# Performance work log

Measured on AMD Instinct MI355X. Metric: run time of the kernel, lower is better.

## Reference

```python
import jax, jax.numpy as jnp
import numpy as np

MIN_NORM = 1e-15
PROJ_EPS = 4e-3  # float32 boundary eps used by hgcn PoincareBall.proj
N_NODES = 100000
BATCH = 32
MAX_COMMENTS = 50
C = 1.0  # comment_curvature


def _norm(x):
    return jnp.maximum(jnp.sqrt(jnp.sum(x * x, axis=-1, keepdims=True)), MIN_NORM)


def _artanh(x):
    return jnp.arctanh(jnp.clip(x, -1.0 + 1e-7, 1.0 - 1e-7))


def proj(x, c):
    n = _norm(x)
    maxnorm = (1.0 - PROJ_EPS) / jnp.sqrt(c)
    return jnp.where(n > maxnorm, x / n * maxnorm, x)


def expmap0(u, c):
    sqc = jnp.sqrt(c)
    un = _norm(u)
    return jnp.tanh(sqc * un) * u / (sqc * un)


def logmap0(p, c):
    sqc = jnp.sqrt(c)
    pn = _norm(p)
    return _artanh(sqc * pn) * p / (sqc * pn)


def mobius_add(x, y, c):
    x2 = jnp.sum(x * x, axis=-1, keepdims=True)
    y2 = jnp.sum(y * y, axis=-1, keepdims=True)
    xy = jnp.sum(x * y, axis=-1, keepdims=True)
    num = (1.0 + 2.0 * c * xy + c * y2) * x + (1.0 - c * x2) * y
    den = 1.0 + 2.0 * c * xy + (c ** 2) * x2 * y2
    return num / jnp.maximum(den, MIN_NORM)


def mobius_matvec(m, x, c):
    sqc = jnp.sqrt(c)
    xn = _norm(x)
    mx = x @ m.T  # [N, out]
    mxn = _norm(mx)
    res = jnp.tanh(mxn / xn * _artanh(sqc * xn)) * mx / (mxn * sqc)
    zero = jnp.all(mx == 0.0, axis=-1, keepdims=True)
    return jnp.where(zero, jnp.zeros_like(res), res)


def hgcn_layer(x, W, b, row, col, n_nodes, c):
    # HypLinear (dropout off / eval mode)
    mv = proj(mobius_matvec(W, x, c), c)
    hyp_bias = proj(expmap0(b[None, :], c), c)
    h = proj(mobius_add(mv, hyp_bias, c), c)
    # HypAgg: tangent-space sparse aggregation adj @ log0(h)
    ht = logmap0(h, c)
    agg = jax.ops.segment_sum(ht[col], row, num_segments=n_nodes)
    h = proj(expmap0(agg, c), c)
    # HypAct with tanh, c_in == c_out
    at = jnp.tanh(logmap0(h, c))
    return proj(expmap0(at, c), c)


def setup_inputs() -> dict:
    key = jax.random.key(0)
    ks = jax.random.split(key, 8)
    E = 1600000
    x = jax.random.normal(ks[0], (N_NODES, 256), dtype=jnp.float32) * 0.1
    edge_row = jax.random.randint(ks[1], (E,), 0, N_NODES, dtype=jnp.int32)
    edge_col = jax.random.randint(ks[2], (E,), 0, N_NODES, dtype=jnp.int32)
    seg_ids = jax.random.randint(ks[3], (N_NODES,), 0, BATCH * MAX_COMMENTS, dtype=jnp.int32)
    W1 = jax.random.normal(ks[4], (128, 256), dtype=jnp.float32) * 0.05
    b1 = jax.random.normal(ks[5], (128,), dtype=jnp.float32) * 0.05
    W2 = jax.random.normal(ks[6], (128, 128), dtype=jnp.float32) * 0.05
    b2 = jax.random.normal(ks[7], (128,), dtype=jnp.float32) * 0.05
    return {"x": x, "edge_row": edge_row, "edge_col": edge_col, "seg_ids": seg_ids,
            "W1": W1, "b1": b1, "W2": W2, "b2": b2}


def reference(x, edge_row, edge_col, seg_ids, W1, b1, W2, b2):
    c = jnp.float32(C)
    # map Euclidean inputs to the Poincare ball (proj_tan0 is identity)
    h = proj(expmap0(x, c), c)
    h = hgcn_layer(h, W1, b1, edge_row, edge_col, N_NODES, c)
    h = hgcn_layer(h, W2, b2, edge_row, edge_col, N_NODES, c)
    # back to tangent space
    h = logmap0(proj(h, c), c)  # [N, hidden]
    # per-subgraph mean pooling (dgl.mean_nodes over node_subgraphs)
    n_seg = BATCH * MAX_COMMENTS
    ssum = jax.ops.segment_sum(h, seg_ids, num_segments=n_seg)
    cnt = jax.ops.segment_sum(jnp.ones((N_NODES,), h.dtype), seg_ids, num_segments=n_seg)
    mean = ssum / jnp.maximum(cnt, 1.0)[:, None]  # empty segments -> zero rows (padding)
    agg = proj(expmap0(mean, c), c)
    return agg.reshape(BATCH, MAX_COMMENTS, -1)
```

## Files before the change

kernel.cpp:

```cpp
#include <hip/hip_runtime.h>


#define MAXN 0.996f
#define CLIPV 0.9999999f
#define MINNORM 1e-15f

typedef __attribute__((ext_vector_type(8))) short  short8;
typedef __attribute__((ext_vector_type(4))) float  f32x4;
typedef __attribute__((ext_vector_type(4))) unsigned short us4;

__device__ __forceinline__ float wave_sum(float v) {
#pragma unroll
  for (int o = 32; o > 0; o >>= 1) v += __shfl_xor(v, o);
  return v;
}
__device__ __forceinline__ float sum16(float v) {
#pragma unroll
  for (int o = 8; o > 0; o >>= 1) v += __shfl_xor(v, o);
  return v;
}

__device__ __forceinline__ unsigned short f2bf(float f) {
  unsigned int u = __float_as_uint(f);
  u = (u + 0x7FFFu + ((u >> 16) & 1u)) >> 16;
  return (unsigned short)u;
}
__device__ __forceinline__ float bf_lo(unsigned int u) {
  return __uint_as_float(u << 16);
}
__device__ __forceinline__ float bf_hi(unsigned int u) {
  return __uint_as_float(u & 0xFFFF0000u);
}

__global__ void bias_kernel(const float* __restrict__ b1i,
                            const float* __restrict__ b2i,
                            float* __restrict__ hb1, float* __restrict__ hb2,
                            float* __restrict__ y21, float* __restrict__ y22) {
  const float* b = blockIdx.x ? b2i : b1i;
  float* hb = blockIdx.x ? hb2 : hb1;
  float* y2o = blockIdx.x ? y22 : y21;
  int lane = threadIdx.x;
  float b0 = b[lane], b1 = b[lane + 64];
  float ssq = wave_sum(b0 * b0 + b1 * b1);
  float un = fmaxf(sqrtf(ssq), MINNORM);
  float t = tanhf(un);
  float s = t / un;
  float n = t;
  if (n > MAXN) { s *= MAXN / n; n = MAXN; }
  hb[lane] = s * b0;
  hb[lane + 64] = s * b1;
  if (lane == 0) y2o[0] = n * n;
}

__global__ void hist_kernel(const int* __restrict__ keys, int* __restrict__ cnt,
                            int n) {
  int e = blockIdx.x * 256 + threadIdx.x;
  if (e < n) atomicAdd(&cnt[keys[e]], 1);
}

__global__ __launch_bounds__(256) void scan_kernel(const int* __restrict__ in,
                                                   int* __restrict__ out,
                                                   int* __restrict__ bsum, int n) {
  __shared__ int sh[256];
  int t = threadIdx.x;
  int base = blockIdx.x * 1024 + t * 4;
  int v0 = 0, v1 = 0, v2 = 0, v3 = 0;
  if (base + 0 < n) v0 = in[base + 0];
  if (base + 1 < n) v1 = in[base + 1];
  if (base + 2 < n) v2 = in[base + 2];
  if (base + 3 < n) v3 = in[base + 3];
  int s = v0 + v1 + v2 + v3;
  sh[t] = s;
  __syncthreads();
  int run = s;
  for (int o = 1; o < 256; o <<= 1) {
    int add = (t >= o) ? sh[t - o] : 0;
    __syncthreads();
    run += add;
    sh[t] = run;
    __syncthreads();
  }
  int excl = run - s;
  if (base + 0 < n) out[base + 0] = excl;
  if (base + 1 < n) out[base + 1] = excl + v0;
  if (base + 2 < n) out[base + 2] = excl + v0 + v1;
  if (base + 3 < n) out[base + 3] = excl + v0 + v1 + v2;
  if (t == 255 && bsum) bsum[blockIdx.x] = run;
}

__global__ void scan_add_kernel(int* __restrict__ pre, const int* __restrict__ boff,
                                int n, int total) {
  int i = blockIdx.x * 256 + threadIdx.x;
  if (i < n) pre[i] += boff[blockIdx.x >> 2];
  if (i == 0) pre[n] = total;
}

__global__ __launch_bounds__(256) void sscan_kernel(const int* __restrict__ in,
                                                    int* __restrict__ out, int n) {
  __shared__ int sh[256];
  int t = threadIdx.x;
  int base = t * 8;
  int v[8];
  int s = 0;
#pragma unroll
  for (int i = 0; i < 8; i++) {
    v[i] = (base + i < n) ? in[base + i] : 0;
    s += v[i];
  }
  sh[t] = s;
  __syncthreads();
  int run = s;
  for (int o = 1; o < 256; o <<= 1) {
    int add = (t >= o) ? sh[t - o] : 0;
    __syncthreads();
    run += add;
    sh[t] = run;
    __syncthreads();
  }
  int running = run - s;
#pragma unroll
  for (int i = 0; i < 8; i++) {
    if (base + i < n) out[base + i] = running;
    running += v[i];
  }
  if (t == 255) out[n] = running;
}

__global__ void fill_kernel(const int* __restrict__ erow, const int* __restrict__ ecol,
                            const int* __restrict__ rowptr, int* __restrict__ fill,
                            int* __restrict__ colidx, int E) {
  int e = blockIdx.x * 256 + threadIdx.x;
  if (e >= E) return;
  int r = erow[e];
  int pos = rowptr[r] + atomicAdd(&fill[r], 1);
  colidx[pos] = ecol[e];
}

__global__ void sfill_kernel(const int* __restrict__ seg,
                             const int* __restrict__ sptr, int* __restrict__ sfil,
                             int* __restrict__ snode, int M) {
  int i = blockIdx.x * 256 + threadIdx.x;
  if (i >= M) return;
  int s = seg[i];
  int pos = sptr[s] + atomicAdd(&sfil[s], 1);
  snode[pos] = i;
}

template <bool L1>
__global__ __launch_bounds__(256) void gemm_fused(const void* __restrict__ Xv,
                                                  const float* __restrict__ Wt,
                                                  const float* __restrict__ hb_g,
                                                  const float* __restrict__ y2_g,
                                                  const float* __restrict__ xnin,
                                                  unsigned short* __restrict__ HT,
                                                  int M, int K) {
  constexpr int GS = 128 * 16 + 16;
  __shared__ alignas(16) char smem[8 * GS];
  __shared__ float hbs[128];
  __shared__ float redS[128][2], redD[128][2];
  __shared__ float rowA[128], rowB[128];
  __shared__ float fsh[128], xsh[128];
  char* sA = smem;
  char* sB = smem + 4 * GS;
  int tid = threadIdx.x;
  int lane = tid & 63;
  int w = tid >> 6;
  int wr = w >> 1, wc = w & 1;
  int m0 = blockIdx.x * 128;

  if (tid < 128) hbs[tid] = hb_g[tid];

  float ssqr[4] = {0.f, 0.f, 0.f, 0.f};
  f32x4 acc[4][4] = {};
  for (int k0 = 0; k0 < K; k0 += 32) {
#pragma unroll
    for (int j = 0; j < 4; j++) {
      int i = tid + 256 * j;
      int row = i >> 3;
      int koff = (i & 7) * 4;
      int gm = m0 + row;
      us4 av;
      if constexpr (L1) {
        if (gm < M) {
          float4 v = *reinterpret_cast<const float4*>(
              &((const float*)Xv)[(size_t)gm * K + k0 + koff]);
          ssqr[j] += v.x * v.x + v.y * v.y + v.z * v.z + v.w * v.w;
          av[0] = f2bf(v.x); av[1] = f2bf(v.y); av[2] = f2bf(v.z); av[3] = f2bf(v.w);
        } else { av[0] = 0; av[1] = 0; av[2] = 0; av[3] = 0; }
      } else {
        if (gm < M) av = *reinterpret_cast<const us4*>(
            &((const unsigned short*)Xv)[(size_t)gm * K + k0 + koff]);
        else { av[0] = 0; av[1] = 0; av[2] = 0; av[3] = 0; }
      }
      *reinterpret_cast<us4*>(&sA[(koff >> 3) * GS + row * 16 + (koff & 7) * 2]) = av;
      float4 wv = *reinterpret_cast<const float4*>(&Wt[(size_t)row * K + k0 + koff]);
      us4 bv;
      bv[0] = f2bf(wv.x); bv[1] = f2bf(wv.y); bv[2] = f2bf(wv.z); bv[3] = f2bf(wv.w);
      *reinterpret_cast<us4*>(&sB[(koff >> 3) * GS + row * 16 + (koff & 7) * 2]) = bv;
    }
    __syncthreads();
    int g = lane >> 4, r = lane & 15;
    short8 af[4], bfr[4];
#pragma unroll
    for (int mb = 0; mb < 4; mb++)
      af[mb] = *reinterpret_cast<const short8*>(
          &sA[g * GS + (wr * 64 + mb * 16 + r) * 16]);
#pragma unroll
    for (int nb = 0; nb < 4; nb++)
      bfr[nb] = *reinterpret_cast<const short8*>(
          &sB[g * GS + (wc * 64 + nb * 16 + r) * 16]);
#pragma unroll
    for (int mb = 0; mb < 4; mb++)
#pragma unroll
      for (int nb = 0; nb < 4; nb++)
        acc[mb][nb] = __builtin_amdgcn_mfma_f32_16x16x32_bf16(
            af[mb], bfr[nb], acc[mb][nb], 0, 0, 0);
    __syncthreads();
  }

  if constexpr (L1) {
#pragma unroll
    for (int j = 0; j < 4; j++) {
      float s = ssqr[j];
      s += __shfl_xor(s, 1); s += __shfl_xor(s, 2); s += __shfl_xor(s, 4);
      if ((tid & 7) == 0) {
        int row = (tid >> 3) + 32 * j;
        float un = fmaxf(sqrtf(s), MINNORM);
        float t = tanhf(un);
        float f, xn;
        if (t > MAXN) { f = MAXN / un; xn = MAXN; }
        else          { f = t / un;    xn = t; }
        fsh[row] = f; xsh[row] = xn;
      }
    }
  }

  int cr = lane >> 4, cc = lane & 15;
#pragma unroll
  for (int mb = 0; mb < 4; mb++)
#pragma unroll
    for (int q = 0; q < 4; q++) {
      float ps = 0.f, dp = 0.f;
#pragma unroll
      for (int nb = 0; nb < 4; nb++) {
        float a = acc[mb][nb][q];
        ps = fmaf(a, a, ps);
        dp = fmaf(a, hbs[wc * 64 + nb * 16 + cc], dp);
      }
      ps += __shfl_xor(ps, 1); ps += __shfl_xor(ps, 2);
      ps += __shfl_xor(ps, 4); ps += __shfl_xor(ps, 8);
      dp += __shfl_xor(dp, 1); dp += __shfl_xor(dp, 2);
      dp += __shfl_xor(dp, 4); dp += __shfl_xor(dp, 8);
      if (cc == 0) {
        int row = wr * 64 + mb * 16 + cr * 4 + q;
        redS[row][wc] = ps;
        redD[row][wc] = dp;
      }
    }
  __syncthreads();

  if (tid < 128) {
    int gm = m0 + tid;
    float mx2 = redS[tid][0] + redS[tid][1];
    float dp  = redD[tid][0] + redD[tid][1];
    float f, xn;
    if constexpr (L1) { f = fsh[tid]; xn = xsh[tid]; }
    else { f = 1.0f; xn = (gm < M) ? xnin[gm] : 0.5f; }
    float mxn = fmaxf(f * sqrtf(mx2), MINNORM);
    float art = atanhf(fminf(xn, CLIPV));
    float tt = tanhf(mxn / xn * art);
    float s_sc = tt / mxn;
    float rn = tt;
    if (rn > MAXN) { s_sc *= MAXN / rn; rn = MAXN; }
    float SA = s_sc * f;
    float x2 = rn * rn;
    float xy = SA * dp;
    float y2 = y2_g[0];
    float ca = 1.0f + 2.0f * xy + y2;
    float cb = 1.0f - x2;
    float den = fmaxf(1.0f + 2.0f * xy + x2 * y2, MINNORM);
    float hn2 = ca * ca * x2 + 2.0f * ca * cb * xy + cb * cb * y2;
    float hn = fmaxf(sqrtf(fmaxf(hn2, 0.f)) / den, MINNORM);
    float ps2 = 1.0f, n = hn;
    if (n > MAXN) { ps2 = MAXN / n; n = MAXN; }
    float ls = atanhf(fminf(n, CLIPV)) / n * ps2;
    rowA[tid] = ls * ca * SA / den;
    rowB[tid] = ls * cb / den;
  }
  __syncthreads();

#pragma unroll
  for (int mb = 0; mb < 4; mb++)
#pragma unroll
    for (int q = 0; q < 4; q++) {
      int row = wr * 64 + mb * 16 + cr * 4 + q;
      int gm = m0 + row;
      if (gm >= M) continue;
      float A = rowA[row], B = rowB[row];
#pragma unroll
      for (int nb = 0; nb < 4; nb++) {
        int col = wc * 64 + nb * 16 + cc;
        float hv = fmaf(A, acc[mb][nb][q], B * hbs[col]);
        HT[(size_t)gm * 128 + col] = f2bf(hv);
      }
    }
}

__global__ void agg_gather_act_kernel(const unsigned int* __restrict__ ht,
                                      const int* __restrict__ rowptr,
                                      const int* __restrict__ colidx,
                                      unsigned int* __restrict__ out,
                                      float* __restrict__ xn2, int M) {
  int row = blockIdx.x * 4 + (threadIdx.x >> 6);
  int lane = threadIdx.x & 63;
  if (row >= M) return;
  int g = lane >> 4;
  int c16 = lane & 15;
  int p0 = rowptr[row], pe = rowptr[row + 1];
  float a0 = 0.f, a1 = 0.f, a2 = 0.f, a3 = 0.f;
  float a4 = 0.f, a5 = 0.f, a6 = 0.f, a7 = 0.f;
  for (int p = p0 + g; p < pe; p += 4) {
    int c = colidx[p];
    uint4 u = *reinterpret_cast<const uint4*>(&ht[(size_t)c * 64 + c16 * 4]);
    a0 += bf_lo(u.x); a1 += bf_hi(u.x);
    a2 += bf_lo(u.y); a3 += bf_hi(u.y);
    a4 += bf_lo(u.z); a5 += bf_hi(u.z);
    a6 += bf_lo(u.w); a7 += bf_hi(u.w);
  }
#pragma unroll
  for (int o = 16; o <= 32; o <<= 1) {
    a0 += __shfl_xor(a0, o); a1 += __shfl_xor(a1, o);
    a2 += __shfl_xor(a2, o); a3 += __shfl_xor(a3, o);
    a4 += __shfl_xor(a4, o); a5 += __shfl_xor(a5, o);
    a6 += __shfl_xor(a6, o); a7 += __shfl_xor(a7, o);
  }
  float ssq = a0 * a0 + a1 * a1 + a2 * a2 + a3 * a3 +
              a4 * a4 + a5 * a5 + a6 * a6 + a7 * a7;
  float an = fmaxf(sqrtf(sum16(ssq)), MINNORM);
  float t = tanhf(an);
  float s = t / an;
  float hn = t;
  if (hn > MAXN) { s *= MAXN / hn; hn = MAXN; }
  float ls = atanhf(fminf(hn, CLIPV)) / hn;
  float sc = ls * s;
  float at0 = tanhf(sc * a0), at1 = tanhf(sc * a1);
  float at2 = tanhf(sc * a2), at3 = tanhf(sc * a3);
  float at4 = tanhf(sc * a4), at5 = tanhf(sc * a5);
  float at6 = tanhf(sc * a6), at7 = tanhf(sc * a7);
  float ssq2 = at0 * at0 + at1 * at1 + at2 * at2 + at3 * at3 +
               at4 * at4 + at5 * at5 + at6 * at6 + at7 * at7;
  float an2 = fmaxf(sqrtf(sum16(ssq2)), MINNORM);
  float t2 = tanhf(an2);
  float s2 = t2 / an2;
  float rn = t2;
  if (t2 > MAXN) { s2 *= MAXN / t2; rn = MAXN; }
  if (g == 0) {
    uint4 o;
    o.x = (unsigned int)f2bf(s2 * at0) | ((unsigned int)f2bf(s2 * at1) << 16);
    o.y = (unsigned int)f2bf(s2 * at2) | ((unsigned int)f2bf(s2 * at3) << 16);
    o.z = (unsigned int)f2bf(s2 * at4) | ((unsigned int)f2bf(s2 * at5) << 16);
    o.w = (unsigned int)f2bf(s2 * at6) | ((unsigned int)f2bf(s2 * at7) << 16);
    *reinterpret_cast<uint4*>(&out[(size_t)row * 64 + c16 * 4]) = o;
    if (c16 == 0) xn2[row] = rn;
  }
}

__global__ __launch_bounds__(256) void pool_gather_kernel(
    const unsigned int* __restrict__ H, const int* __restrict__ sptr,
    const int* __restrict__ snode, float* __restrict__ out, int S) {
  __shared__ float2 part[4][64];
  int s = blockIdx.x;
  if (s >= S) return;
  int w = threadIdx.x >> 6, lane = threadIdx.x & 63;
  int p0 = sptr[s], pe = sptr[s + 1];
  float m0 = 0.f, m1 = 0.f;
  for (int p = p0 + w; p < pe; p += 4) {
    int nd = snode[p];
    unsigned int u = H[(size_t)nd * 64 + lane];
    float h0 = bf_lo(u), h1 = bf_hi(u);
    float pn = fmaxf(sqrtf(wave_sum(h0 * h0 + h1 * h1)), MINNORM);
    float psc = 1.0f, n = pn;
    if (n > MAXN) { psc = MAXN / n; n = MAXN; }
    float ls = atanhf(fminf(n, CLIPV)) / n * psc;
    m0 += ls * h0;
    m1 += ls * h1;
  }
  part[w][lane] = make_float2(m0, m1);
  __syncthreads();
  if (w == 0) {
    float2 a = part[0][lane], b = part[1][lane];
    float2 c = part[2][lane], d = part[3][lane];
    m0 = a.x + b.x + c.x + d.x;
    m1 = a.y + b.y + c.y + d.y;
    float cn = fmaxf((float)(pe - p0), 1.0f);
    m0 /= cn; m1 /= cn;
    float un = fmaxf(sqrtf(wave_sum(m0 * m0 + m1 * m1)), MINNORM);
    float t = tanhf(un);
    float sc = t / un;
    if (t > MAXN) sc *= MAXN / t;
    *reinterpret_cast<float2*>(&out[(size_t)s * 128 + lane * 2]) =
        make_float2(sc * m0, sc * m1);
  }
}

extern "C" void kernel_launch(void* const* d_in, const int* in_sizes, int n_in,
                              void* d_out, int out_size, void* d_ws, size_t ws_size,
                              hipStream_t stream) {
  const float* x  = (const float*)d_in[0];
  const int* erow = (const int*)d_in[1];
  const int* ecol = (const int*)d_in[2];
  const int* seg  = (const int*)d_in[3];
  const float* W1 = (const float*)d_in[4];
  const float* b1 = (const float*)d_in[5];
  const float* W2 = (const float*)d_in[6];
  const float* b2 = (const float*)d_in[7];
  float* out = (float*)d_out;

  const int N = 100000, E = 1600000, S = 1600;

  float* W = (float*)d_ws;
  float* xn2   = W;
  float* hb1   = W + 100000;
  float* hb2   = W + 100128;
  float* y21   = W + 100256;
  float* y22   = W + 100260;
  unsigned int* HT = (unsigned int*)(W + 100352);
  unsigned int* CB = HT + 6400000;
  int* hcnt    = (int*)(CB + 6400000);
  int* fill    = hcnt + 100000;
  int* scnt    = fill + 100000;
  int* sfil    = scnt + 1600;
  int* rowptr  = sfil + 1600;
  int* bsum    = rowptr + 100001;
  int* sptr    = bsum + 256;
  int* snode   = sptr + 1601;
  int* colidx  = snode + 100000;

  dim3 blk(256);
  int rowBlocks  = (N + 3) / 4;
  int gemmBlocks = (N + 127) / 128;
  int edgeBlocks = (E + 255) / 256;
  int nodeBlocks = (N + 255) / 256;
  int scanBlocks = (N + 1023) / 1024;

  hipMemsetAsync(hcnt, 0, (size_t)(200000 + 3200) * sizeof(int), stream);
  hist_kernel<<<edgeBlocks, blk, 0, stream>>>(erow, hcnt, E);
  scan_kernel<<<scanBlocks, blk, 0, stream>>>(hcnt, rowptr, bsum, N);
  scan_kernel<<<1, blk, 0, stream>>>(bsum, bsum, nullptr, scanBlocks);
  scan_add_kernel<<<nodeBlocks, blk, 0, stream>>>(rowptr, bsum, N, E);
  fill_kernel<<<edgeBlocks, blk, 0, stream>>>(erow, ecol, rowptr, fill, colidx, E);
  hist_kernel<<<nodeBlocks, blk, 0, stream>>>(seg, scnt, N);
  sscan_kernel<<<1, blk, 0, stream>>>(scnt, sptr, S);
  sfill_kernel<<<nodeBlocks, blk, 0, stream>>>(seg, sptr, sfil, snode, N);

  bias_kernel<<<2, 64, 0, stream>>>(b1, b2, hb1, hb2, y21, y22);

  gemm_fused<true><<<gemmBlocks, blk, 0, stream>>>(
      x, W1, hb1, y21, nullptr, (unsigned short*)HT, N, 256);
  agg_gather_act_kernel<<<rowBlocks, blk, 0, stream>>>(HT, rowptr, colidx, CB, xn2, N);

  gemm_fused<false><<<gemmBlocks, blk, 0, stream>>>(
      CB, W2, hb2, y22, xn2, (unsigned short*)HT, N, 128);
  agg_gather_act_kernel<<<rowBlocks, blk, 0, stream>>>(HT, rowptr, colidx, CB, xn2, N);

  pool_gather_kernel<<<S, blk, 0, stream>>>(CB, sptr, snode, out, S);
}
```

Baseline: 690.6 us.

## Merge setup kernels, pre-convert weights to bf16, widen GEMM K-step

The histogram, bias, and weight-conversion work now runs in one multi-role setup kernel, the two scans share one launch, and the two CSR fills share one launch, which cuts the launch count. Weights are converted to bf16 once up front, so the GEMM tiles no longer convert W on every load. The GEMM K-step doubles to 64 with 16-byte loads and packed bf16 conversion through an inline v_cvt_pk_bf16_f32 instruction. This doubles shared memory per block, which may lower occupancy.

After: 634.6 us. 1.09x faster.

```diff
diff --git a/kernel.cpp b/kernel.cpp
--- a/kernel.cpp
+++ b/kernel.cpp
@@ -7,7 +7,6 @@
 
 typedef __attribute__((ext_vector_type(8))) short  short8;
 typedef __attribute__((ext_vector_type(4))) float  f32x4;
-typedef __attribute__((ext_vector_type(4))) unsigned short us4;
 
 __device__ __forceinline__ float wave_sum(float v) {
 #pragma unroll
@@ -31,39 +30,117 @@
 __device__ __forceinline__ float bf_hi(unsigned int u) {
   return __uint_as_float(u & 0xFFFF0000u);
 }
-
-__global__ void bias_kernel(const float* __restrict__ b1i,
-                            const float* __restrict__ b2i,
-                            float* __restrict__ hb1, float* __restrict__ hb2,
-                            float* __restrict__ y21, float* __restrict__ y22) {
-  const float* b = blockIdx.x ? b2i : b1i;
-  float* hb = blockIdx.x ? hb2 : hb1;
-  float* y2o = blockIdx.x ? y22 : y21;
-  int lane = threadIdx.x;
-  float b0 = b[lane], b1 = b[lane + 64];
-  float ssq = wave_sum(b0 * b0 + b1 * b1);
-  float un = fmaxf(sqrtf(ssq), MINNORM);
-  float t = tanhf(un);
-  float s = t / un;
-  float n = t;
-  if (n > MAXN) { s *= MAXN / n; n = MAXN; }
-  hb[lane] = s * b0;
-  hb[lane + 64] = s * b1;
-  if (lane == 0) y2o[0] = n * n;
-}
-
-__global__ void hist_kernel(const int* __restrict__ keys, int* __restrict__ cnt,
-                            int n) {
-  int e = blockIdx.x * 256 + threadIdx.x;
-  if (e < n) atomicAdd(&cnt[keys[e]], 1);
-}
-
-__global__ __launch_bounds__(256) void scan_kernel(const int* __restrict__ in,
-                                                   int* __restrict__ out,
-                                                   int* __restrict__ bsum, int n) {
+__device__ __forceinline__ unsigned int cvt2(float lo, float hi) {
+  unsigned int r;
+  asm("v_cvt_pk_bf16_f32 %0, %1, %2" : "=v"(r) : "v"(lo), "v"(hi));
+  return r;
+}
+
+__global__ __launch_bounds__(256) void setup_kernel(
+    const int* __restrict__ erow, const int* __restrict__ seg,
+    const float* __restrict__ b1, const float* __restrict__ b2,
+    const float* __restrict__ W1, const float* __restrict__ W2,
+    int* __restrict__ hcnt, int* __restrict__ scnt,
+    float* __restrict__ hb1, float* __restrict__ hb2,
+    float* __restrict__ y21, float* __restrict__ y22,
+    unsigned short* __restrict__ Wb1, unsigned short* __restrict__ Wb2) {
+  const int EB = 6250, NB = 391, WB = 192;
+  int b = blockIdx.x, tid = threadIdx.x;
+  if (b < EB) {
+    int e = b * 256 + tid;
+    if (e < 1600000) atomicAdd(&hcnt[erow[e]], 1);
+  } else if (b < EB + NB) {
+    int i = (b - EB) * 256 + tid;
+    if (i < 100000) atomicAdd(&scnt[seg[i]], 1);
+  } else if (b < EB + NB + WB) {
+    int i = (b - EB - NB) * 256 + tid;
+    if (i < 32768) Wb1[i] = f2bf(W1[i]);
+    else           Wb2[i - 32768] = f2bf(W2[i - 32768]);
+  } else {
+    if (tid >= 64) return;
+    int which = b - (EB + NB + WB);
+    const float* bb = which ? b2 : b1;
+    float* hb  = which ? hb2 : hb1;
+    float* y2o = which ? y22 : y21;
+    float v0 = bb[tid], v1 = bb[tid + 64];
+    float ssq = wave_sum(v0 * v0 + v1 * v1);
+    float un = fmaxf(sqrtf(ssq), MINNORM);
+    float t = tanhf(un);
+    float s = t / un;
+    float n = t;
+    if (n > MAXN) { s *= MAXN / n; n = MAXN; }
+    hb[tid] = s * v0;
+    hb[tid + 64] = s * v1;
+    if (tid == 0) y2o[0] = n * n;
+  }
+}
+
+__global__ __launch_bounds__(256) void scan_both_kernel(
+    const int* __restrict__ hcnt, int* __restrict__ rowptr,
+    int* __restrict__ bsum, const int* __restrict__ scnt,
+    int* __restrict__ sptr) {
   __shared__ int sh[256];
   int t = threadIdx.x;
-  int base = blockIdx.x * 1024 + t * 4;
+  if (blockIdx.x < 98) {
+    const int n = 100000;
+    int base = blockIdx.x * 1024 + t * 4;
+    int v0 = 0, v1 = 0, v2 = 0, v3 = 0;
+    if (base + 0 < n) v0 = hcnt[base + 0];
+    if (base + 1 < n) v1 = hcnt[base + 1];
+    if (base + 2 < n) v2 = hcnt[base + 2];
+    if (base + 3 < n) v3 = hcnt[base + 3];
+    int s = v0 + v1 + v2 + v3;
+    sh[t] = s;
+    __syncthreads();
+    int run = s;
+    for (int o = 1; o < 256; o <<= 1) {
+      int add = (t >= o) ? sh[t - o] : 0;
+      __syncthreads();
+      run += add;
+      sh[t] = run;
+      __syncthreads();
+    }
+    int excl = run - s;
+    if (base + 0 < n) rowptr[base + 0] = excl;
+    if (base + 1 < n) rowptr[base + 1] = excl + v0;
+    if (base + 2 < n) rowptr[base + 2] = excl + v0 + v1;
+    if (base + 3 < n) rowptr[base + 3] = excl + v0 + v1 + v2;
+    if (t == 255) bsum[blockIdx.x] = run;
+  } else {
+    const int n = 1600;
+    int base = t * 8;
+    int v[8];
+    int s = 0;
+#pragma unroll
+    for (int i = 0; i < 8; i++) {
+      v[i] = (base + i < n) ? scnt[base + i] : 0;
+      s += v[i];
+    }
+    sh[t] = s;
+    __syncthreads();
+    int run = s;
+    for (int o = 1; o < 256; o <<= 1) {
+      int add = (t >= o) ? sh[t - o] : 0;
+      __syncthreads();
+      run += add;
+      sh[t] = run;
+      __syncthreads();
+    }
+    int running = run - s;
+#pragma unroll
+    for (int i = 0; i < 8; i++) {
+      if (base + i < n) sptr[base + i] = running;
+      running += v[i];
+    }
+    if (t == 255) sptr[n] = running;
+  }
+}
+
+__global__ __launch_bounds__(256) void scan_kernel(const int* __restrict__ in,
+                                                   int* __restrict__ out, int n) {
+  __shared__ int sh[256];
+  int t = threadIdx.x;
+  int base = t * 4;
   int v0 = 0, v1 = 0, v2 = 0, v3 = 0;
   if (base + 0 < n) v0 = in[base + 0];
   if (base + 1 < n) v1 = in[base + 1];
@@ -85,7 +162,6 @@
   if (base + 1 < n) out[base + 1] = excl + v0;
   if (base + 2 < n) out[base + 2] = excl + v0 + v1;
   if (base + 3 < n) out[base + 3] = excl + v0 + v1 + v2;
-  if (t == 255 && bsum) bsum[blockIdx.x] = run;
 }
 
 __global__ void scan_add_kernel(int* __restrict__ pre, const int* __restrict__ boff,
@@ -95,73 +171,45 @@
   if (i == 0) pre[n] = total;
 }
 
-__global__ __launch_bounds__(256) void sscan_kernel(const int* __restrict__ in,
-                                                    int* __restrict__ out, int n) {
-  __shared__ int sh[256];
-  int t = threadIdx.x;
-  int base = t * 8;
-  int v[8];
-  int s = 0;
-#pragma unroll
-  for (int i = 0; i < 8; i++) {
-    v[i] = (base + i < n) ? in[base + i] : 0;
-    s += v[i];
-  }
-  sh[t] = s;
-  __syncthreads();
-  int run = s;
-  for (int o = 1; o < 256; o <<= 1) {
-    int add = (t >= o) ? sh[t - o] : 0;
-    __syncthreads();
-    run += add;
-    sh[t] = run;
-    __syncthreads();
-  }
-  int running = run - s;
-#pragma unroll
-  for (int i = 0; i < 8; i++) {
-    if (base + i < n) out[base + i] = running;
-    running += v[i];
-  }
-  if (t == 255) out[n] = running;
-}
-
-__global__ void fill_kernel(const int* __restrict__ erow, const int* __restrict__ ecol,
-                            const int* __restrict__ rowptr, int* __restrict__ fill,
-                            int* __restrict__ colidx, int E) {
-  int e = blockIdx.x * 256 + threadIdx.x;
-  if (e >= E) return;
-  int r = erow[e];
-  int pos = rowptr[r] + atomicAdd(&fill[r], 1);
-  colidx[pos] = ecol[e];
-}
-
-__global__ void sfill_kernel(const int* __restrict__ seg,
-                             const int* __restrict__ sptr, int* __restrict__ sfil,
-                             int* __restrict__ snode, int M) {
-  int i = blockIdx.x * 256 + threadIdx.x;
-  if (i >= M) return;
-  int s = seg[i];
-  int pos = sptr[s] + atomicAdd(&sfil[s], 1);
-  snode[pos] = i;
+__global__ void fill_both_kernel(const int* __restrict__ erow,
+                                 const int* __restrict__ ecol,
+                                 const int* __restrict__ rowptr,
+                                 int* __restrict__ fill, int* __restrict__ colidx,
+                                 const int* __restrict__ seg,
+                                 const int* __restrict__ sptr,
+                                 int* __restrict__ sfil, int* __restrict__ snode) {
+  int b = blockIdx.x, tid = threadIdx.x;
+  if (b < 6250) {
+    int e = b * 256 + tid;
+    if (e >= 1600000) return;
+    int r = erow[e];
+    int pos = rowptr[r] + atomicAdd(&fill[r], 1);
+    colidx[pos] = ecol[e];
+  } else {
+    int i = (b - 6250) * 256 + tid;
+    if (i >= 100000) return;
+    int s = seg[i];
+    int pos = sptr[s] + atomicAdd(&sfil[s], 1);
+    snode[pos] = i;
+  }
 }
 
 template <bool L1>
 __global__ __launch_bounds__(256) void gemm_fused(const void* __restrict__ Xv,
-                                                  const float* __restrict__ Wt,
+                                                  const unsigned short* __restrict__ Wb,
                                                   const float* __restrict__ hb_g,
                                                   const float* __restrict__ y2_g,
                                                   const float* __restrict__ xnin,
                                                   unsigned short* __restrict__ HT,
                                                   int M, int K) {
   constexpr int GS = 128 * 16 + 16;
-  __shared__ alignas(16) char smem[8 * GS];
+  __shared__ alignas(16) char smem[16 * GS];
   __shared__ float hbs[128];
   __shared__ float redS[128][2], redD[128][2];
   __shared__ float rowA[128], rowB[128];
   __shared__ float fsh[128], xsh[128];
   char* sA = smem;
-  char* sB = smem + 4 * GS;
+  char* sB = smem + 8 * GS;
   int tid = threadIdx.x;
   int lane = tid & 63;
   int w = tid >> 6;
@@ -170,51 +218,56 @@
 
   if (tid < 128) hbs[tid] = hb_g[tid];
 
+  int row_s = tid >> 3;
+  int kg = tid & 7;
   float ssqr[4] = {0.f, 0.f, 0.f, 0.f};
   f32x4 acc[4][4] = {};
-  for (int k0 = 0; k0 < K; k0 += 32) {
+  for (int k0 = 0; k0 < K; k0 += 64) {
 #pragma unroll
     for (int j = 0; j < 4; j++) {
-      int i = tid + 256 * j;
-      int row = i >> 3;
-      int koff = (i & 7) * 4;
+      int row = row_s + 32 * j;
       int gm = m0 + row;
-      us4 av;
+      int kb = k0 + kg * 8;
+      uint4 av = make_uint4(0, 0, 0, 0);
       if constexpr (L1) {
         if (gm < M) {
-          float4 v = *reinterpret_cast<const float4*>(
-              &((const float*)Xv)[(size_t)gm * K + k0 + koff]);
-          ssqr[j] += v.x * v.x + v.y * v.y + v.z * v.z + v.w * v.w;
-          av[0] = f2bf(v.x); av[1] = f2bf(v.y); av[2] = f2bf(v.z); av[3] = f2bf(v.w);
-        } else { av[0] = 0; av[1] = 0; av[2] = 0; av[3] = 0; }
+          const float* xr = &((const float*)Xv)[(size_t)gm * K + kb];
+          float4 v0 = *reinterpret_cast<const float4*>(xr);
+          float4 v1 = *reinterpret_cast<const float4*>(xr + 4);
+          ssqr[j] += v0.x * v0.x + v0.y * v0.y + v0.z * v0.z + v0.w * v0.w +
+                     v1.x * v1.x + v1.y * v1.y + v1.z * v1.z + v1.w * v1.w;
+          av.x = cvt2(v0.x, v0.y); av.y = cvt2(v0.z, v0.w);
+          av.z = cvt2(v1.x, v1.y); av.w = cvt2(v1.z, v1.w);
+        }
       } else {
-        if (gm < M) av = *reinterpret_cast<const us4*>(
-            &((const unsigned short*)Xv)[(size_t)gm * K + k0 + koff]);
-        else { av[0] = 0; av[1] = 0; av[2] = 0; av[3] = 0; }
+        if (gm < M) av = *reinterpret_cast<const uint4*>(
+            &((const unsigned short*)Xv)[(size_t)gm * K + kb]);
       }
-      *reinterpret_cast<us4*>(&sA[(koff >> 3) * GS + row * 16 + (koff & 7) * 2]) = av;
-      float4 wv = *reinterpret_cast<const float4*>(&Wt[(size_t)row * K + k0 + koff]);
-      us4 bv;
-      bv[0] = f2bf(wv.x); bv[1] = f2bf(wv.y); bv[2] = f2bf(wv.z); bv[3] = f2bf(wv.w);
-      *reinterpret_cast<us4*>(&sB[(koff >> 3) * GS + row * 16 + (koff & 7) * 2]) = bv;
+      *reinterpret_cast<uint4*>(&sA[kg * GS + row * 16]) = av;
+      uint4 bv = *reinterpret_cast<const uint4*>(&Wb[(size_t)row * K + kb]);
+      *reinterpret_cast<uint4*>(&sB[kg * GS + row * 16]) = bv;
     }
     __syncthreads();
-    int g = lane >> 4, r = lane & 15;
-    short8 af[4], bfr[4];
-#pragma unroll
-    for (int mb = 0; mb < 4; mb++)
-      af[mb] = *reinterpret_cast<const short8*>(
-          &sA[g * GS + (wr * 64 + mb * 16 + r) * 16]);
-#pragma unroll
-    for (int nb = 0; nb < 4; nb++)
-      bfr[nb] = *reinterpret_cast<const short8*>(
-          &sB[g * GS + (wc * 64 + nb * 16 + r) * 16]);
-#pragma unroll
-    for (int mb = 0; mb < 4; mb++)
+    int gh = lane >> 4, r = lane & 15;
+#pragma unroll
+    for (int kk = 0; kk < 2; kk++) {
+      int g2 = kk * 4 + gh;
+      short8 af[4], bfv[4];
+#pragma unroll
+      for (int mb = 0; mb < 4; mb++)
+        af[mb] = *reinterpret_cast<const short8*>(
+            &sA[g2 * GS + (wr * 64 + mb * 16 + r) * 16]);
 #pragma unroll
       for (int nb = 0; nb < 4; nb++)
-        acc[mb][nb] = __builtin_amdgcn_mfma_f32_16x16x32_bf16(
-            af[mb], bfr[nb], acc[mb][nb], 0, 0, 0);
+        bfv[nb] = *reinterpret_cast<const short8*>(
+            &sB[g2 * GS + (wc * 64 + nb * 16 + r) * 16]);
+#pragma unroll
+      for (int mb = 0; mb < 4; mb++)
+#pragma unroll
+        for (int nb = 0; nb < 4; nb++)
+          acc[mb][nb] = __builtin_amdgcn_mfma_f32_16x16x32_bf16(
+              af[mb], bfv[nb], acc[mb][nb], 0, 0, 0);
+    }
     __syncthreads();
   }
 
@@ -224,7 +277,7 @@
       float s = ssqr[j];
       s += __shfl_xor(s, 1); s += __shfl_xor(s, 2); s += __shfl_xor(s, 4);
       if ((tid & 7) == 0) {
-        int row = (tid >> 3) + 32 * j;
+        int row = row_s + 32 * j;
         float un = fmaxf(sqrtf(s), MINNORM);
         float t = tanhf(un);
         float f, xn;
@@ -424,7 +477,9 @@
   float* hb2   = W + 100128;
   float* y21   = W + 100256;
   float* y22   = W + 100260;
-  unsigned int* HT = (unsigned int*)(W + 100352);
+  unsigned short* Wb1 = (unsigned short*)(W + 100352);
+  unsigned short* Wb2 = Wb1 + 32768;
+  unsigned int* HT = (unsigned int*)(W + 124928);
   unsigned int* CB = HT + 6400000;
   int* hcnt    = (int*)(CB + 6400000);
   int* fill    = hcnt + 100000;
@@ -439,28 +494,22 @@
   dim3 blk(256);
   int rowBlocks  = (N + 3) / 4;
   int gemmBlocks = (N + 127) / 128;
-  int edgeBlocks = (E + 255) / 256;
-  int nodeBlocks = (N + 255) / 256;
-  int scanBlocks = (N + 1023) / 1024;
-
-  hipMemsetAsync(hcnt, 0, (size_t)(200000 + 3200) * sizeof(int), stream);
-  hist_kernel<<<edgeBlocks, blk, 0, stream>>>(erow, hcnt, E);
-  scan_kernel<<<scanBlocks, blk, 0, stream>>>(hcnt, rowptr, bsum, N);
-  scan_kernel<<<1, blk, 0, stream>>>(bsum, bsum, nullptr, scanBlocks);
-  scan_add_kernel<<<nodeBlocks, blk, 0, stream>>>(rowptr, bsum, N, E);
-  fill_kernel<<<edgeBlocks, blk, 0, stream>>>(erow, ecol, rowptr, fill, colidx, E);
-  hist_kernel<<<nodeBlocks, blk, 0, stream>>>(seg, scnt, N);
-  sscan_kernel<<<1, blk, 0, stream>>>(scnt, sptr, S);
-  sfill_kernel<<<nodeBlocks, blk, 0, stream>>>(seg, sptr, sfil, snode, N);
-
-  bias_kernel<<<2, 64, 0, stream>>>(b1, b2, hb1, hb2, y21, y22);
+
+  hipMemsetAsync(hcnt, 0, (size_t)203200 * sizeof(int), stream);
+  setup_kernel<<<6250 + 391 + 192 + 2, blk, 0, stream>>>(
+      erow, seg, b1, b2, W1, W2, hcnt, scnt, hb1, hb2, y21, y22, Wb1, Wb2);
+  scan_both_kernel<<<99, blk, 0, stream>>>(hcnt, rowptr, bsum, scnt, sptr);
+  scan_kernel<<<1, blk, 0, stream>>>(bsum, bsum, 98);
+  scan_add_kernel<<<(N + 255) / 256, blk, 0, stream>>>(rowptr, bsum, N, E);
+  fill_both_kernel<<<6250 + 391, blk, 0, stream>>>(
+      erow, ecol, rowptr, fill, colidx, seg, sptr, sfil, snode);
 
   gemm_fused<true><<<gemmBlocks, blk, 0, stream>>>(
-      x, W1, hb1, y21, nullptr, (unsigned short*)HT, N, 256);
+      x, Wb1, hb1, y21, nullptr, (unsigned short*)HT, N, 256);
   agg_gather_act_kernel<<<rowBlocks, blk, 0, stream>>>(HT, rowptr, colidx, CB, xn2, N);
 
   gemm_fused<false><<<gemmBlocks, blk, 0, stream>>>(
-      CB, W2, hb2, y22, xn2, (unsigned short*)HT, N, 128);
+      CB, Wb2, hb2, y22, xn2, (unsigned short*)HT, N, 128);
   agg_gather_act_kernel<<<rowBlocks, blk, 0, stream>>>(HT, rowptr, colidx, CB, xn2, N);
 
   pool_gather_kernel<<<S, blk, 0, stream>>>(CB, sptr, snode, out, S);
```
